# Kernel tuning notes

Hardware: AMD Instinct MI355X
Metric: run time of the kernel (lower is better)

The kernel has to match this reference:

```python
import jax, jax.numpy as jnp
import numpy as np

B, H, L, N = 16, 256, 4096, 64  # N = d_state//2 retained complex-conjugate modes (S4D)
EPS = 1e-5


def setup_inputs() -> dict:
    key = jax.random.key(0)
    ks = jax.random.split(key, 6)
    x = jax.random.normal(ks[0], (B, H, L), dtype=jnp.float32)
    # dt log-uniform in [1e-3, 1e-1] per channel (standard S4 init)
    log_dt = (jax.random.uniform(ks[1], (H,), dtype=jnp.float32)
              * (np.log(0.1) - np.log(0.001)) + np.log(0.001))
    # S4D-Lin init: A_n = -1/2 + i*pi*n
    A_re = -0.5 * jnp.ones((H, N), dtype=jnp.float32)
    A_im = jnp.pi * jnp.broadcast_to(jnp.arange(N, dtype=jnp.float32), (H, N))
    # bidirectional -> 2 channel groups of C
    C_re = jax.random.normal(ks[2], (2, H, N), dtype=jnp.float32)
    C_im = jax.random.normal(ks[3], (2, H, N), dtype=jnp.float32)
    D = jax.random.normal(ks[4], (H,), dtype=jnp.float32)
    ln_w = jnp.ones((H,), dtype=jnp.float32)
    ln_b = jnp.zeros((H,), dtype=jnp.float32)
    W_out = jax.random.normal(ks[5], (H, H), dtype=jnp.float32) / np.sqrt(H)
    b_out = jnp.zeros((H,), dtype=jnp.float32)
    return {"x": x, "log_dt": log_dt, "A_re": A_re, "A_im": A_im,
            "C_re": C_re, "C_im": C_im, "D": D,
            "ln_w": ln_w, "ln_b": ln_b, "W_out": W_out, "b_out": b_out}


def _s4_forward(x, log_dt, A_re, A_im, C_re, C_im, D, ln_w, ln_b, W_out, b_out):
    # LayerNorm over channel dim (x.transpose -> LN(d_model) -> transpose back)
    mu = jnp.mean(x, axis=1, keepdims=True)
    var = jnp.mean((x - mu) ** 2, axis=1, keepdims=True)
    z = (x - mu) * jax.lax.rsqrt(var + EPS) * ln_w[None, :, None] + ln_b[None, :, None]

    # --- S4D kernel via Vandermonde (ZOH-style discretization) ---
    A = A_re + 1j * A_im                         # (H, N)
    C = C_re + 1j * C_im                         # (2, H, N)
    dt = jnp.exp(log_dt)[:, None]                # (H, 1)
    dtA = dt * A                                 # (H, N)
    C_t = C * (jnp.exp(dtA) - 1.0) / A           # (2, H, N)
    t = jnp.arange(L, dtype=jnp.float32)
    V = jnp.exp(dtA[:, :, None] * t)             # (H, N, L) Vandermonde
    K = 2.0 * jnp.real(jnp.einsum('dhn,hnl->dhl', C_t, V))  # (2, H, L)

    # bidirectional: forward kernel padded right, backward kernel flipped, padded left
    k = jnp.pad(K[0], ((0, 0), (0, L))) + jnp.pad(K[1][:, ::-1], ((0, 0), (L, 0)))

    # FFT convolution over length 2L
    Uf = jnp.fft.rfft(z, n=2 * L)                # (B, H, L+1)
    Kf = jnp.fft.rfft(k, n=2 * L)                # (H, L+1)
    y = jnp.fft.irfft(Uf * Kf[None], n=2 * L)[..., :L]

    y = y + D[None, :, None] * z                 # skip D*u
    y = jax.nn.gelu(y)                           # S4 default activation
    # transposed position-wise output linear (postact=None -> plain Linear)
    y = jnp.einsum('oh,bhl->bol', W_out, y) + b_out[None, :, None]
    return x + y                                  # residual


def reference(x, log_dt, A_re, A_im, C_re, C_im, D, ln_w, ln_b, W_out, b_out):
    return _s4_forward(x, log_dt, A_re, A_im, C_re, C_im, D, ln_w, ln_b, W_out, b_out)
```

## Files before the change

### kernel.cpp

```cpp
#include <hip/hip_runtime.h>
#include <math.h>

#define B_ 16
#define H_ 256
#define L_ 4096
#define N_ 64
#define HN (H_*N_)
#define HL (H_*L_)
#define BHL (B_*H_*L_)
#define SPAD 64

#define WVT_OFS 0
#define TM_OFS  8192
#define E2T_OFS 12288
#define MATS_PER 20480

typedef short bf16x8 __attribute__((ext_vector_type(8)));
typedef float f32x4  __attribute__((ext_vector_type(4)));

__device__ __forceinline__ unsigned int pk2(float a, float b) {
    return ((__float_as_uint(a) + 0x8000u) >> 16) |
           ((__float_as_uint(b) + 0x8000u) & 0xffff0000u);
}
__device__ __forceinline__ unsigned short bfr(float a) {
    return (unsigned short)((__float_as_uint(a) + 0x8000u) >> 16);
}
__device__ __forceinline__ float ubf(unsigned short u) {
    return __uint_as_float(((unsigned int)u) << 16);
}

__global__ void __launch_bounds__(64) mats_kernel(const float* __restrict__ log_dt,
                                                  const float* __restrict__ A_re,
                                                  const float* __restrict__ A_im,
                                                  const float* __restrict__ C_re,
                                                  const float* __restrict__ C_im,
                                                  const float* __restrict__ D,
                                                  unsigned short* __restrict__ mats,
                                                  float2* __restrict__ Wc) {
    int hd = blockIdx.x;
    int h = hd >> 1, d = hd & 1;
    int m = threadIdx.x;
    __shared__ float2 pws[65 * 64];
    __shared__ float2 c2s[64];
    __shared__ float  Karr[64];

    int i = h * 64 + m;
    float dt = expf(log_dt[h]);
    float Are = A_re[i], Aim = A_im[i];
    float dr = dt * Are, di = dt * Aim;
    float er = expf(dr);
    float wr = er * cosf(di), wi = er * sinf(di);
    float em1r = wr - 1.0f, em1i = wi;
    float inv = 1.0f / (Are * Are + Aim * Aim);
    float qr = (em1r * Are + em1i * Aim) * inv;
    float qi = (em1i * Are - em1r * Aim) * inv;
    float Cr = C_re[d * HN + i], Ci = C_im[d * HN + i];
    float2 c2;
    c2.x = 2.0f * (Cr * qr - Ci * qi);
    c2.y = 2.0f * (Cr * qi + Ci * qr);
    c2s[m] = c2;
    float pr = 1.0f, pi = 0.0f;
    for (int k = 0; k < 64; ++k) {
        float2 p; p.x = pr; p.y = pi;
        pws[k * 64 + ((m + k) & 63)] = p;
        float t = pr * wr - pi * wi;
        pi = pr * wi + pi * wr;
        pr = t;
    }
    {
        float2 p; p.x = pr; p.y = pi;
        pws[64 * 64 + ((m + 64) & 63)] = p;
        Wc[hd * 64 + m] = p;
    }
    __syncthreads();
    {
        float kk = 0.f;
        for (int mm = 0; mm < 64; ++mm) {
            float2 c = c2s[mm];
            float2 pw = pws[m * 64 + ((mm + m) & 63)];
            kk += c.x * pw.x - c.y * pw.y;
        }
        Karr[m] = kk;
    }
    __syncthreads();
    float dh = D[h];
    unsigned short* mb = mats + (size_t)hd * MATS_PER;
    for (int i2 = 0; i2 < 32; ++i2) {
        int e0 = 2 * i2, e1 = e0 + 1;
        int k0 = d ? e0 : 63 - e0;
        int k1 = d ? e1 : 63 - e1;
        float2 p0 = pws[k0 * 64 + ((m + k0) & 63)];
        float2 p1 = pws[k1 * 64 + ((m + k1) & 63)];
        *(unsigned int*)(mb + WVT_OFS + (2 * m) * 64 + e0)     = pk2(p0.x, p1.x);
        *(unsigned int*)(mb + WVT_OFS + (2 * m + 1) * 64 + e0) = pk2(p0.y, p1.y);
    }
    for (int i2 = 0; i2 < 32; ++i2) {
        int e0 = 2 * i2, e1 = e0 + 1;
        float v0, v1;
        if (d == 0) {
            v0 = (e0 <= m) ? Karr[m - e0] : 0.f;
            v1 = (e1 <= m) ? Karr[m - e1] : 0.f;
            if (e0 == m) v0 += dh;
            if (e1 == m) v1 += dh;
        } else {
            v0 = (e0 > m) ? Karr[e0 - m - 1] : 0.f;
            v1 = (e1 > m) ? Karr[e1 - m - 1] : 0.f;
        }
        *(unsigned int*)(mb + TM_OFS + m * 64 + e0) = pk2(v0, v1);
    }
    {
        int kp = d ? (63 - m) : (m + 1);
        for (int mm = 0; mm < 64; ++mm) {
            float2 c = c2s[mm];
            float2 pw = pws[kp * 64 + ((mm + kp) & 63)];
            float vr = c.x * pw.x - c.y * pw.y;
            float vi = -(c.x * pw.y + c.y * pw.x);
            *(unsigned int*)(mb + E2T_OFS + m * 128 + 2 * mm) = pk2(vr, vi);
        }
    }
}

__global__ void __launch_bounds__(256) wbf_kernel(const float* __restrict__ W,
                                                  unsigned short* __restrict__ Wbf) {
    int i = (blockIdx.x * 256 + threadIdx.x) * 4;
    float4 v = *(const float4*)(W + i);
    uint2 u;
    u.x = pk2(v.x, v.y);
    u.y = pk2(v.z, v.w);
    *(uint2*)(Wbf + i) = u;
}

__global__ void __launch_bounds__(256) ln_kernel(const float* __restrict__ x,
                                                 const float* __restrict__ lnw,
                                                 const float* __restrict__ lnb,
                                                 unsigned short* __restrict__ zb,
                                                 unsigned short* __restrict__ xbf) {
    int b  = blockIdx.y;
    int l0 = blockIdx.x * 256;
    int t  = threadIdx.x;
    int hq = t >> 6, lo = t & 63;
    int l  = l0 + lo * 4;
    __shared__ float4 r1[4][64];
    __shared__ float4 r2[4][64];
    __shared__ float4 muS[64];
    __shared__ float4 rsS[64];
    const float* xb = x + (size_t)b * HL;
    float4 s1 = {0.f,0.f,0.f,0.f}, s2 = {0.f,0.f,0.f,0.f};
    #pragma unroll 4
    for (int hh = 0; hh < 64; ++hh) {
        int h = hq * 64 + hh;
        float4 v = *(const float4*)(xb + (size_t)h * L_ + l);
        s1.x += v.x; s1.y += v.y; s1.z += v.z; s1.w += v.w;
        s2.x += v.x*v.x; s2.y += v.y*v.y; s2.z += v.z*v.z; s2.w += v.w*v.w;
    }
    r1[hq][lo] = s1; r2[hq][lo] = s2;
    __syncthreads();
    if (t < 64) {
        float4 S1 = r1[0][t], S2 = r2[0][t];
        #pragma unroll
        for (int q = 1; q < 4; ++q) {
            float4 a = r1[q][t], c = r2[q][t];
            S1.x += a.x; S1.y += a.y; S1.z += a.z; S1.w += a.w;
            S2.x += c.x; S2.y += c.y; S2.z += c.z; S2.w += c.w;
        }
        const float invH = 1.0f / 256.0f;
        float4 mu, rs;
        mu.x = S1.x*invH; mu.y = S1.y*invH; mu.z = S1.z*invH; mu.w = S1.w*invH;
        rs.x = rsqrtf(S2.x*invH - mu.x*mu.x + 1e-5f);
        rs.y = rsqrtf(S2.y*invH - mu.y*mu.y + 1e-5f);
        rs.z = rsqrtf(S2.z*invH - mu.z*mu.z + 1e-5f);
        rs.w = rsqrtf(S2.w*invH - mu.w*mu.w + 1e-5f);
        muS[t] = mu; rsS[t] = rs;
    }
    __syncthreads();
    float4 mu = muS[lo], rs = rsS[lo];
    #pragma unroll 4
    for (int hh = 0; hh < 64; ++hh) {
        int h = hq * 64 + hh;
        float w = lnw[h], bb = lnb[h];
        float4 v = *(const float4*)(xb + (size_t)h * L_ + l);
        float4 zz;
        zz.x = (v.x - mu.x) * rs.x * w + bb;
        zz.y = (v.y - mu.y) * rs.y * w + bb;
        zz.z = (v.z - mu.z) * rs.z * w + bb;
        zz.w = (v.w - mu.w) * rs.w * w + bb;
        uint2 u;
        u.x = pk2(zz.x, zz.y);
        u.y = pk2(zz.z, zz.w);
        *(uint2*)(zb + (size_t)b * HL + (size_t)h * L_ + l) = u;
        uint2 ux;
        ux.x = pk2(v.x, v.y);
        ux.y = pk2(v.z, v.w);
        *(uint2*)(xbf + (size_t)b * HL + (size_t)h * L_ + l) = ux;
    }
}

#define MFMA16(a,b,c) __builtin_amdgcn_mfma_f32_16x16x32_bf16((a),(b),(c),0,0,0)

__global__ void __launch_bounds__(128, 3) ssm_kernel(const unsigned short* __restrict__ zb,
                                                     const unsigned short* __restrict__ mats,
                                                     const float2* __restrict__ Wc,
                                                     unsigned short* __restrict__ y2) {
    int bhd = blockIdx.x;
    int d  = bhd & 1;
    int bh = bhd >> 1;
    int h  = bh & (H_ - 1);
    int t  = threadIdx.x;
    int w  = t >> 6, l = t & 63;
    int p  = w;

    __shared__ __align__(16) char smem[16384];
    char* sUd = smem;

    const unsigned short* mb = mats + (size_t)(h * 2 + d) * MATS_PER;

    {
        const char* zrow = (const char*)(zb + (size_t)bh * L_);
        #pragma unroll
        for (int k = 0; k < 4; ++k) {
            int row = w * 32 + k * 8 + (l >> 3);
            int chunk = (l & 7) ^ (row & 7);
            const char* src = zrow + row * 128 + chunk * 16;
            __builtin_amdgcn_global_load_lds(
                (const __attribute__((address_space(1))) unsigned int*)src,
                (__attribute__((address_space(3))) unsigned int*)(smem + w * 4096 + k * 1024),
                16, 0, 0);
        }
    }
    __syncthreads();

    bf16x8 za[4][2];
    int arow = l & 15;
    int koff = (l >> 4) * 8;
    #pragma unroll
    for (int cb = 0; cb < 4; ++cb) {
        int row = cb * 16 + arow;
        unsigned int sw = (row & 7) << 4;
        #pragma unroll
        for (int kb = 0; kb < 2; ++kb) {
            unsigned int byte = (unsigned)(row * 128 + (kb * 32 + koff) * 2) ^ sw;
            za[cb][kb] = *(bf16x8*)(smem + byte);
        }
    }
    asm volatile("s_waitcnt lgkmcnt(0)" ::: "memory");
    __syncthreads();

    #pragma unroll
    for (int mcb = 0; mcb < 4; ++mcb) {
        int mcblk = p * 4 + mcb;
        const unsigned short* wv = mb + WVT_OFS + (mcblk * 16 + arow) * 64 + koff;
        bf16x8 b0 = *(const bf16x8*)(wv);
        bf16x8 b1 = *(const bf16x8*)(wv + 32);
        #pragma unroll
        for (int cb = 0; cb < 4; ++cb) {
            f32x4 acc = {0.f, 0.f, 0.f, 0.f};
            acc = MFMA16(za[cb][0], b0, acc);
            acc = MFMA16(za[cb][1], b1, acc);
            int mc = mcblk * 16 + arow;
            #pragma unroll
            for (int rr = 0; rr < 4; ++rr) {
                int c = cb * 16 + (l >> 4) * 4 + rr;
                unsigned int byte = ((unsigned)(c * 256 + mc * 2)) ^ ((c & 7) << 4);
                *(unsigned short*)(sUd + byte) = bfr(acc[rr]);
            }
        }
    }
    __syncthreads();

    if (p == 0) {
        float2 w64 = Wc[(h * 2 + d) * 64 + l];
        float sr = 0.f, si = 0.f;
        if (d == 0) {
            for (int c = 0; c < 64; ++c) {
                unsigned int byte = ((unsigned)(c * 256 + l * 4)) ^ ((c & 7) << 4);
                unsigned int uu = *(unsigned int*)(sUd + byte);
                float ur = __uint_as_float(uu << 16);
                float ui = __uint_as_float(uu & 0xffff0000u);
                *(unsigned int*)(sUd + byte) = pk2(sr, si);
                float nsr = fmaf(w64.x, sr, fmaf(-w64.y, si, ur));
                float nsi = fmaf(w64.x, si, fmaf(w64.y, sr, ui));
                sr = nsr; si = nsi;
            }
        } else {
            for (int c = 63; c >= 0; --c) {
                unsigned int byte = ((unsigned)(c * 256 + l * 4)) ^ ((c & 7) << 4);
                unsigned int uu = *(unsigned int*)(sUd + byte);
                float ur = __uint_as_float(uu << 16);
                float ui = __uint_as_float(uu & 0xffff0000u);
                *(unsigned int*)(sUd + byte) = pk2(sr, si);
                float nsr = fmaf(w64.x, sr, fmaf(-w64.y, si, ur));
                float nsi = fmaf(w64.x, si, fmaf(w64.y, sr, ui));
                sr = nsr; si = nsi;
            }
        }
    }
    __syncthreads();

    f32x4 yacc[2][4];
    #pragma unroll
    for (int jb = 0; jb < 2; ++jb) {
        int jblk = p * 2 + jb;
        const unsigned short* tm = mb + TM_OFS + (jblk * 16 + arow) * 64 + koff;
        bf16x8 tb0 = *(const bf16x8*)(tm);
        bf16x8 tb1 = *(const bf16x8*)(tm + 32);
        const unsigned short* et = mb + E2T_OFS + (jblk * 16 + arow) * 128 + koff;
        bf16x8 eb0 = *(const bf16x8*)(et);
        bf16x8 eb1 = *(const bf16x8*)(et + 32);
        bf16x8 eb2 = *(const bf16x8*)(et + 64);
        bf16x8 eb3 = *(const bf16x8*)(et + 96);
        #pragma unroll
        for (int cb = 0; cb < 4; ++cb) {
            f32x4 acc = {0.f, 0.f, 0.f, 0.f};
            acc = MFMA16(za[cb][0], tb0, acc);
            acc = MFMA16(za[cb][1], tb1, acc);
            int row = cb * 16 + arow;
            unsigned int sw = (row & 7) << 4;
            bf16x8 sa0 = *(bf16x8*)(sUd + (((unsigned)(row * 256 + (0 * 32 + koff) * 2)) ^ sw));
            bf16x8 sa1 = *(bf16x8*)(sUd + (((unsigned)(row * 256 + (1 * 32 + koff) * 2)) ^ sw));
            bf16x8 sa2 = *(bf16x8*)(sUd + (((unsigned)(row * 256 + (2 * 32 + koff) * 2)) ^ sw));
            bf16x8 sa3 = *(bf16x8*)(sUd + (((unsigned)(row * 256 + (3 * 32 + koff) * 2)) ^ sw));
            acc = MFMA16(sa0, eb0, acc);
            acc = MFMA16(sa1, eb1, acc);
            acc = MFMA16(sa2, eb2, acc);
            acc = MFMA16(sa3, eb3, acc);
            yacc[jb][cb] = acc;
        }
    }
    __syncthreads();

    {
        #pragma unroll
        for (int jb = 0; jb < 2; ++jb) {
            int j = (p * 2 + jb) * 16 + arow;
            #pragma unroll
            for (int cb = 0; cb < 4; ++cb) {
                #pragma unroll
                for (int rr = 0; rr < 4; ++rr) {
                    int c = cb * 16 + (l >> 4) * 4 + rr;
                    unsigned int byte = ((unsigned)(c * 128 + j * 2)) ^ ((c & 7) << 4);
                    *(unsigned short*)(smem + byte) = bfr(yacc[jb][cb][rr]);
                }
            }
        }
    }
    __syncthreads();
    {
        int row = t >> 1, halfq = t & 1;
        unsigned int rsw = (row & 7) << 4;
        char* go = (char*)(y2 + ((size_t)bh * 2 + d) * L_);
        #pragma unroll
        for (int j = 0; j < 4; ++j) {
            unsigned int off = (unsigned)(row * 128 + halfq * 64 + j * 16);
            uint4 a = *(const uint4*)(smem + (off ^ rsw));
            *(uint4*)(go + off) = a;
        }
    }
}

__global__ void __launch_bounds__(256, 3) outproj_kernel(
        const unsigned short* __restrict__ y2,
        const unsigned short* __restrict__ Wbf,
        const unsigned short* __restrict__ xbf,
        const float* __restrict__ bias,
        float* __restrict__ out) {
    int b  = blockIdx.z;
    int o0 = blockIdx.y * 128;
    int l0 = blockIdx.x * 128;
    int t  = threadIdx.x;
    int w  = t >> 6, lane = t & 63;
    int wr = w >> 1, wc = w & 1;
    int l15 = lane & 15, q = lane >> 4;

    __shared__ __align__(16) char lds[34816];
    unsigned short* At = (unsigned short*)lds;
    unsigned short* Bt = (unsigned short*)(lds + 16384);

    f32x4 acc[4][4];
    #pragma unroll
    for (int i = 0; i < 4; ++i)
        #pragma unroll
        for (int j = 0; j < 4; ++j) acc[i][j] = (f32x4){0.f, 0.f, 0.f, 0.f};

    const unsigned short* Wb0 = Wbf + (size_t)o0 * 256;
    unsigned int swz = (unsigned)(l15 & 7) << 4;

    int h_loc = t >> 2, lq = t & 3;

    for (int kt = 0; kt < 4; ++kt) {
        int k0 = kt * 64;
        {
            const unsigned short* yb0 =
                y2 + (((size_t)b * H_ + k0 + h_loc) * 2) * L_ + l0 + lq * 32;
            uint4 f[4], g[4];
            #pragma unroll
            for (int j = 0; j < 4; ++j) f[j] = *(const uint4*)(yb0 + j * 8);
            #pragma unroll
            for (int j = 0; j < 4; ++j) g[j] = *(const uint4*)(yb0 + L_ + j * 8);
            #pragma unroll
            for (int j = 0; j < 4; ++j) {
                #pragma unroll
                for (int e = 0; e < 8; ++e) {
                    int l_loc = lq * 32 + j * 8 + e;
                    float y = ubf(((const unsigned short*)&f[j])[e]) +
                              ubf(((const unsigned short*)&g[j])[e]);
                    float inner = 0.7978845608028654f * (y + 0.044715f * y * y * y);
                    float en = __expf(-2.0f * inner);
                    float gv = y * __builtin_amdgcn_rcpf(1.0f + en);
                    *(unsigned short*)((char*)At +
                        (((unsigned)(l_loc * 128 + h_loc * 2)) ^ ((l_loc & 7) << 4))) = bfr(gv);
                }
            }
        }
        #pragma unroll
        for (int s = 0; s < 4; ++s) {
            int id = (w * 4 + s) * 64 + lane;
            int row = id >> 3, ch = id & 7;
            int chl = ch ^ (row & 7);
            uint4 vb = *(const uint4*)(Wb0 + (size_t)row * 256 + k0 + chl * 8);
            *(uint4*)(Bt + id * 8) = vb;
        }
        __syncthreads();
        #pragma unroll
        for (int kk = 0; kk < 2; ++kk) {
            bf16x8 af[4], bfr_[4];
            #pragma unroll
            for (int rb = 0; rb < 4; ++rb) {
                int li = wr * 64 + rb * 16 + l15;
                af[rb] = *(const bf16x8*)((char*)At + li * 128 + (((kk * 64 + q * 16)) ^ swz));
                int oi = wc * 64 + rb * 16 + l15;
                bfr_[rb] = *(const bf16x8*)((char*)Bt + oi * 128 + (((kk * 64 + q * 16)) ^ swz));
            }
            #pragma unroll
            for (int rb = 0; rb < 4; ++rb)
                #pragma unroll
                for (int cb = 0; cb < 4; ++cb)
                    acc[rb][cb] = MFMA16(af[rb], bfr_[cb], acc[rb][cb]);
        }
        __syncthreads();
    }

    float* Eb = (float*)lds;
    for (int pp = 0; pp < 2; ++pp) {
        if (wc == pp) {
            #pragma unroll
            for (int cb = 0; cb < 4; ++cb) {
                int o_loc = cb * 16 + l15;
                unsigned int esw = (unsigned)(o_loc & 7) << 4;
                #pragma unroll
                for (int rb = 0; rb < 4; ++rb) {
                    int colbase = wr * 64 + rb * 16 + q * 4;
                    #pragma unroll
                    for (int r = 0; r < 4; ++r) {
                        int col = colbase + r;
                        *(float*)((char*)Eb + o_loc * 528 + (((unsigned)(col * 4)) ^ esw)) =
                            acc[rb][cb][r];
                    }
                }
            }
        }
        __syncthreads();
        int o_loc = t >> 2, lseg = t & 3;
        int o = o0 + pp * 64 + o_loc;
        float bo = bias[o];
        unsigned int esw = (unsigned)(o_loc & 7) << 4;
        size_t off = ((size_t)b * H_ + o) * L_ + l0 + lseg * 32;
        const unsigned short* xr = xbf + off;
        float* orow = out + off;
        #pragma unroll
        for (int j = 0; j < 8; ++j) {
            float4 e = *(const float4*)((char*)Eb + o_loc * 528 +
                                        (((unsigned)(lseg * 128 + j * 16)) ^ esw));
            uint2 xv2 = *(const uint2*)(xr + j * 4);
            float4 ov;
            ov.x = ubf((unsigned short)(xv2.x & 0xffffu))  + bo + e.x;
            ov.y = ubf((unsigned short)(xv2.x >> 16))      + bo + e.y;
            ov.z = ubf((unsigned short)(xv2.y & 0xffffu))  + bo + e.z;
            ov.w = ubf((unsigned short)(xv2.y >> 16))      + bo + e.w;
            *(float4*)(orow + j * 4) = ov;
        }
        __syncthreads();
    }
}

extern "C" void kernel_launch(void* const* d_in, const int* in_sizes, int n_in,
                              void* d_out, int out_size, void* d_ws, size_t ws_size,
                              hipStream_t stream) {
    const float* x      = (const float*)d_in[0];
    const float* log_dt = (const float*)d_in[1];
    const float* A_re   = (const float*)d_in[2];
    const float* A_im   = (const float*)d_in[3];
    const float* C_re   = (const float*)d_in[4];
    const float* C_im   = (const float*)d_in[5];
    const float* D      = (const float*)d_in[6];
    const float* lnw    = (const float*)d_in[7];
    const float* lnb    = (const float*)d_in[8];
    const float* W      = (const float*)d_in[9];
    const float* bout   = (const float*)d_in[10];
    float* out = (float*)d_out;

    unsigned short* zb   = (unsigned short*)d_ws;
    unsigned short* y2   = zb + (size_t)BHL + SPAD;
    unsigned short* xbf  = y2 + 2 * (size_t)BHL + SPAD;
    unsigned short* mats = xbf + (size_t)BHL + SPAD;
    float2* Wc = (float2*)(mats + 512 * (size_t)MATS_PER);
    unsigned short* Wbf = (unsigned short*)(Wc + 512 * 64);

    mats_kernel<<<512, 64, 0, stream>>>(log_dt, A_re, A_im, C_re, C_im, D, mats, Wc);
    wbf_kernel<<<64, 256, 0, stream>>>(W, Wbf);
    ln_kernel<<<dim3(L_ / 256, B_), 256, 0, stream>>>(x, lnw, lnb, zb, xbf);
    ssm_kernel<<<B_ * H_ * 2, 128, 0, stream>>>(zb, mats, Wc, y2);
    outproj_kernel<<<dim3(L_ / 128, H_ / 128, B_), 256, 0, stream>>>(y2, Wbf, xbf, bout, out);
}
```

Baseline: 194.5 us.

## Retile output projection to cover all 256 outputs per block, avoiding duplicate GELU work

The output projection block now covers 64 sequence positions and all 256 output channels, with each wave owning 64 outputs, instead of a 128x128 tile. Before, each input tile was loaded and put through GELU twice, once per output-channel half. Now it is computed once per block, which removes redundant global reads of y2 and redundant transcendental work. In exchange, each block loads the full 256-row weight slice every k-step, uses more LDS (40KB), and writes its epilogue in four serialized passes. The grid is 1024 blocks instead of 1024 in 3D, so the block count is unchanged.

```diff
diff --git a/kernel.cpp b/kernel.cpp
--- a/kernel.cpp
+++ b/kernel.cpp
@@ -363,17 +363,15 @@
         const unsigned short* __restrict__ xbf,
         const float* __restrict__ bias,
         float* __restrict__ out) {
-    int b  = blockIdx.z;
-    int o0 = blockIdx.y * 128;
-    int l0 = blockIdx.x * 128;
+    int b  = blockIdx.y;
+    int l0 = blockIdx.x * 64;
     int t  = threadIdx.x;
     int w  = t >> 6, lane = t & 63;
-    int wr = w >> 1, wc = w & 1;
     int l15 = lane & 15, q = lane >> 4;
 
-    __shared__ __align__(16) char lds[34816];
+    __shared__ __align__(16) char lds[40960];
     unsigned short* At = (unsigned short*)lds;
-    unsigned short* Bt = (unsigned short*)(lds + 16384);
+    unsigned short* Bt = (unsigned short*)(lds + 8192);
 
     f32x4 acc[4][4];
     #pragma unroll
@@ -381,7 +379,6 @@
         #pragma unroll
         for (int j = 0; j < 4; ++j) acc[i][j] = (f32x4){0.f, 0.f, 0.f, 0.f};
 
-    const unsigned short* Wb0 = Wbf + (size_t)o0 * 256;
     unsigned int swz = (unsigned)(l15 & 7) << 4;
 
     int h_loc = t >> 2, lq = t & 3;
@@ -390,33 +387,34 @@
         int k0 = kt * 64;
         {
             const unsigned short* yb0 =
-                y2 + (((size_t)b * H_ + k0 + h_loc) * 2) * L_ + l0 + lq * 32;
-            uint4 f[4], g[4];
+                y2 + (((size_t)b * H_ + k0 + h_loc) * 2) * L_ + l0 + lq * 16;
+            uint4 f0 = *(const uint4*)(yb0);
+            uint4 f1 = *(const uint4*)(yb0 + 8);
+            uint4 g0 = *(const uint4*)(yb0 + L_);
+            uint4 g1 = *(const uint4*)(yb0 + L_ + 8);
             #pragma unroll
-            for (int j = 0; j < 4; ++j) f[j] = *(const uint4*)(yb0 + j * 8);
-            #pragma unroll
-            for (int j = 0; j < 4; ++j) g[j] = *(const uint4*)(yb0 + L_ + j * 8);
-            #pragma unroll
-            for (int j = 0; j < 4; ++j) {
+            for (int j = 0; j < 2; ++j) {
+                uint4 fv = j ? f1 : f0;
+                uint4 gv = j ? g1 : g0;
                 #pragma unroll
                 for (int e = 0; e < 8; ++e) {
-                    int l_loc = lq * 32 + j * 8 + e;
-                    float y = ubf(((const unsigned short*)&f[j])[e]) +
-                              ubf(((const unsigned short*)&g[j])[e]);
+                    int l_loc = lq * 16 + j * 8 + e;
+                    float y = ubf(((const unsigned short*)&fv)[e]) +
+                              ubf(((const unsigned short*)&gv)[e]);
                     float inner = 0.7978845608028654f * (y + 0.044715f * y * y * y);
                     float en = __expf(-2.0f * inner);
-                    float gv = y * __builtin_amdgcn_rcpf(1.0f + en);
+                    float gvv = y * __builtin_amdgcn_rcpf(1.0f + en);
                     *(unsigned short*)((char*)At +
-                        (((unsigned)(l_loc * 128 + h_loc * 2)) ^ ((l_loc & 7) << 4))) = bfr(gv);
+                        (((unsigned)(l_loc * 128 + h_loc * 2)) ^ ((l_loc & 7) << 4))) = bfr(gvv);
                 }
             }
         }
         #pragma unroll
-        for (int s = 0; s < 4; ++s) {
-            int id = (w * 4 + s) * 64 + lane;
+        for (int s = 0; s < 8; ++s) {
+            int id = s * 256 + t;
             int row = id >> 3, ch = id & 7;
             int chl = ch ^ (row & 7);
-            uint4 vb = *(const uint4*)(Wb0 + (size_t)row * 256 + k0 + chl * 8);
+            uint4 vb = *(const uint4*)(Wbf + (size_t)row * 256 + k0 + chl * 8);
             *(uint4*)(Bt + id * 8) = vb;
         }
         __syncthreads();
@@ -425,9 +423,9 @@
             bf16x8 af[4], bfr_[4];
             #pragma unroll
             for (int rb = 0; rb < 4; ++rb) {
-                int li = wr * 64 + rb * 16 + l15;
+                int li = rb * 16 + l15;
                 af[rb] = *(const bf16x8*)((char*)At + li * 128 + (((kk * 64 + q * 16)) ^ swz));
-                int oi = wc * 64 + rb * 16 + l15;
+                int oi = w * 64 + rb * 16 + l15;
                 bfr_[rb] = *(const bf16x8*)((char*)Bt + oi * 128 + (((kk * 64 + q * 16)) ^ swz));
             }
             #pragma unroll
@@ -440,15 +438,15 @@
     }
 
     float* Eb = (float*)lds;
-    for (int pp = 0; pp < 2; ++pp) {
-        if (wc == pp) {
+    for (int pp = 0; pp < 4; ++pp) {
+        if (w == pp) {
             #pragma unroll
             for (int cb = 0; cb < 4; ++cb) {
                 int o_loc = cb * 16 + l15;
                 unsigned int esw = (unsigned)(o_loc & 7) << 4;
                 #pragma unroll
                 for (int rb = 0; rb < 4; ++rb) {
-                    int colbase = wr * 64 + rb * 16 + q * 4;
+                    int colbase = rb * 16 + q * 4;
                     #pragma unroll
                     for (int r = 0; r < 4; ++r) {
                         int col = colbase + r;
@@ -460,16 +458,16 @@
         }
         __syncthreads();
         int o_loc = t >> 2, lseg = t & 3;
-        int o = o0 + pp * 64 + o_loc;
+        int o = pp * 64 + o_loc;
         float bo = bias[o];
         unsigned int esw = (unsigned)(o_loc & 7) << 4;
-        size_t off = ((size_t)b * H_ + o) * L_ + l0 + lseg * 32;
+        size_t off = ((size_t)b * H_ + o) * L_ + l0 + lseg * 16;
         const unsigned short* xr = xbf + off;
         float* orow = out + off;
         #pragma unroll
-        for (int j = 0; j < 8; ++j) {
+        for (int j = 0; j < 4; ++j) {
             float4 e = *(const float4*)((char*)Eb + o_loc * 528 +
-                                        (((unsigned)(lseg * 128 + j * 16)) ^ esw));
+                                        (((unsigned)(lseg * 64 + j * 16)) ^ esw));
             uint2 xv2 = *(const uint2*)(xr + j * 4);
             float4 ov;
             ov.x = ubf((unsigned short)(xv2.x & 0xffffu))  + bo + e.x;
@@ -509,5 +507,5 @@
     wbf_kernel<<<64, 256, 0, stream>>>(W, Wbf);
     ln_kernel<<<dim3(L_ / 256, B_), 256, 0, stream>>>(x, lnw, lnb, zb, xbf);
     ssm_kernel<<<B_ * H_ * 2, 128, 0, stream>>>(zb, mats, Wc, y2);
-    outproj_kernel<<<dim3(L_ / 128, H_ / 128, B_), 256, 0, stream>>>(y2, Wbf, xbf, bout, out);
-}
+    outproj_kernel<<<dim3(L_ / 64, B_), 256, 0, stream>>>(y2, Wbf, xbf, bout, out);
+}
```

Result: no change. 193.2 us (-0.6%).
